# Optimization experiments

Hardware: AMD Instinct MI355X
Metric: run time of the kernel (lower is better)

## Reference

```python
import jax, jax.numpy as jnp
import numpy as np

B = 256   # batch size
NX = 256  # spatial grid points
T = 100   # time steps in u
TEMP = 1.0
LAM = 0.9  # lambda_1


def _advection(u, dt, dx, coeff):
    d = (jnp.roll(u, 1, axis=1) - jnp.roll(u, -1, axis=1)) * u
    return coeff[:, None, None] * dt[:, None, None] * d / (2.0 * dx[:, None, None])


def _diffusion(u, dt, dx, coeff):
    d = jnp.roll(u, 1, axis=1) + jnp.roll(u, -1, axis=1) - 2.0 * u
    return -(coeff[:, None, None] * dt[:, None, None] * d / dx[:, None, None] ** 2)


def _linear_advection(u, dt, dx, coeff):
    num = u - jnp.roll(u, -1, axis=1)
    return -coeff[:, None, None] * dt[:, None, None] * num / dx[:, None, None]


def _anchored_l2(xi, xj, ui, uj, dt, dx, coeff):
    # us[i, j, :] = ui[j, :, -1] - uj[i, :, -2]  -> [2B, 2B, NX]
    us = ui[..., -1][None, :, :] - uj[..., -2][:, None, :]
    adv = _advection(xi, dt, dx, coeff[:, 0])
    diff = _diffusion(xi, dt, dx, coeff[:, 1])
    dis = _linear_advection(xi, dt, dx, coeff[:, 2])
    updates = (adv + diff + dis)[..., 0]  # [2B, NX]
    pd = (xi[..., 0] + updates)[:, None, :] - xj[..., 0][None, :, :]  # [2B, 2B, NX]
    d = us - pd
    return jnp.sum(d * d, axis=-1)  # norm(dim=-1)**2


def reference(x1, x2, u, dt, dx, vs):
    bs = x1.shape[0]
    # _pde_similarity(vs): pairwise sqrt(sum|vi*vj|) / max(||vi||, ||vj||)
    prod = jnp.sqrt(jnp.sum(jnp.abs(vs[None, :, :] * vs[:, None, :]), axis=-1))
    nv = jnp.linalg.norm(vs, axis=-1)
    sim = prod / jnp.maximum(nv[:, None], nv[None, :])
    ss = jnp.nan_to_num(1.0 - LAM * sim, nan=0.0)
    # drop diagonal (row-major, static indices), then tile to [2B, 2(B-1)]
    ri, ci = np.nonzero(~np.eye(bs, dtype=bool))
    ss = ss[ri, ci].reshape(bs, bs - 1)
    ss = jnp.tile(ss, (2, 2))
    reps = jnp.concatenate([x2, x1], axis=0)           # [2B, NX, 1, 1]
    reps = reps.reshape(2 * bs, -1, reps.shape[-1])    # flatten(1,2) -> [2B, NX, 1]
    u2 = jnp.concatenate([u, u], axis=0)
    dt2 = jnp.concatenate([dt, dt], axis=0)
    vs2 = jnp.concatenate([vs, vs], axis=0)
    simmat = _anchored_l2(reps, reps, u2, u2, dt2, dx, vs2)  # [2B, 2B]
    l_pos = jnp.diagonal(simmat, offset=bs)
    r_pos = jnp.diagonal(simmat, offset=-bs)
    pos = jnp.concatenate([l_pos, r_pos]).reshape(2 * bs, 1)
    m = np.eye(2 * bs) + np.eye(2 * bs, k=-bs) + np.eye(2 * bs, k=bs)
    nri, nci = np.nonzero((1 - m).astype(bool))
    neg = simmat[nri, nci].reshape(2 * bs, 2 * bs - 2) * ss
    logits = jnp.concatenate([pos, neg], axis=1) / TEMP
    lp = jax.nn.log_softmax(logits, axis=-1)
    # CrossEntropyLoss(reduction='sum') with all labels == 0
    return -jnp.sum(lp[:, 0]) / (2 * bs)


def setup_inputs():
    key = jax.random.key(0)
    k1, k2, k3, k4, k5 = jax.random.split(key, 5)
    return {
        'x1': jax.random.normal(k1, (B, NX, 1, 1), dtype=jnp.float32),
        'x2': jax.random.normal(k2, (B, NX, 1, 1), dtype=jnp.float32),
        'u': jax.random.normal(k3, (B, NX, T), dtype=jnp.float32),
        'dt': jax.random.uniform(k4, (B,), dtype=jnp.float32),
        'dx': jnp.ones((1,), dtype=jnp.float32),
        'vs': jax.random.normal(k5, (B, 3), dtype=jnp.float32),
    }
```

## Files before the change

### kernel.cpp

```cpp
#include <hip/hip_runtime.h>
#include <math.h>

#define BQ 256
#define NXQ 256
#define TQ 100
#define N2 512
#define TILE 32
#define PITCH 257

__global__ __launch_bounds__(256) void prep_kernel(
    const float* __restrict__ x1, const float* __restrict__ x2,
    const float* __restrict__ u, const float* __restrict__ dt,
    const float* __restrict__ dx, const float* __restrict__ vs,
    float* __restrict__ A, float* __restrict__ C, float* __restrict__ SS) {
  int blk = blockIdx.x;
  int t = threadIdx.x;
  if (blk < N2) {
    int r = blk;
    int b = r & (BQ - 1);
    const float* xr = (r < BQ ? x2 : x1);
    __shared__ float ws[NXQ];
    ws[t] = xr[b * NXQ + t];
    __syncthreads();
    float w0 = ws[t];
    float wm = ws[(t + NXQ - 1) & (NXQ - 1)];
    float wp = ws[(t + 1) & (NXQ - 1)];
    float dtv = dt[b];
    float dxv = dx[0];
    float c0 = vs[b * 3 + 0], c1 = vs[b * 3 + 1], c2 = vs[b * 3 + 2];
    float adv = c0 * dtv * (wm - wp) * w0 / (2.0f * dxv);
    float dif = -(c1 * dtv * (wm + wp - 2.0f * w0) / (dxv * dxv));
    float dis = -c2 * dtv * (w0 - wp) / dxv;
    float upd = adv + dif + dis;
    const float* urow = u + (size_t)(b * NXQ + t) * TQ;
    A[r * NXQ + t] = urow[TQ - 1] + w0;
    C[r * NXQ + t] = urow[TQ - 2] + w0 + upd;
  } else {
    int i = blk - N2;
    int j = t;
    float vi0 = vs[i * 3], vi1 = vs[i * 3 + 1], vi2 = vs[i * 3 + 2];
    float vj0 = vs[j * 3], vj1 = vs[j * 3 + 1], vj2 = vs[j * 3 + 2];
    float nvi = sqrtf(vi0 * vi0 + vi1 * vi1 + vi2 * vi2);
    float nvj = sqrtf(vj0 * vj0 + vj1 * vj1 + vj2 * vj2);
    float prod = sqrtf(fabsf(vi0 * vj0) + fabsf(vi1 * vj1) + fabsf(vi2 * vj2));
    float sim = prod / fmaxf(nvi, nvj);
    float ssv = 1.0f - 0.9f * sim;
    if (isnan(ssv)) ssv = 0.0f;
    SS[i * BQ + j] = ssv;
  }
}

__global__ __launch_bounds__(256) void dist_kernel(const float* __restrict__ A,
                                                   const float* __restrict__ C,
                                                   float* __restrict__ SIM) {
  __shared__ float At[TILE * PITCH];
  __shared__ float Ct[TILE * PITCH];
  int t = threadIdx.x;
  int i0 = blockIdx.y * TILE;
  int j0 = blockIdx.x * TILE;
  for (int k = 0; k < TILE * NXQ / 256; k++) {
    int idx = k * 256 + t;
    int row = idx >> 8;
    int col = idx & (NXQ - 1);
    At[row * PITCH + col] = A[(j0 + row) * NXQ + col];
    Ct[row * PITCH + col] = C[(i0 + row) * NXQ + col];
  }
  __syncthreads();
  int ii = t >> 3;
  int jj = (t & 7) << 2;
  float acc0 = 0.f, acc1 = 0.f, acc2 = 0.f, acc3 = 0.f;
  for (int x = 0; x < NXQ; x++) {
    float cv = Ct[ii * PITCH + x];
    float d0 = At[(jj + 0) * PITCH + x] - cv;
    float d1 = At[(jj + 1) * PITCH + x] - cv;
    float d2 = At[(jj + 2) * PITCH + x] - cv;
    float d3 = At[(jj + 3) * PITCH + x] - cv;
    acc0 = fmaf(d0, d0, acc0);
    acc1 = fmaf(d1, d1, acc1);
    acc2 = fmaf(d2, d2, acc2);
    acc3 = fmaf(d3, d3, acc3);
  }
  float4 v = make_float4(acc0, acc1, acc2, acc3);
  *(float4*)&SIM[(i0 + ii) * N2 + j0 + jj] = v;
}

__global__ __launch_bounds__(256) void row_kernel(const float* __restrict__ SIM,
                                                  const float* __restrict__ SS,
                                                  double* __restrict__ ROW) {
  int r = blockIdx.x;
  int t = threadIdx.x;
  int rb = r & (BQ - 1);
  int jstar = (r + BQ) & (N2 - 1);
  float posval = SIM[r * N2 + jstar];
  float ssv = SS[rb * BQ + t];
  float v0, v1;
  {
    int j = t;
    if (j == jstar)                  v0 = posval;
    else if ((j & (BQ - 1)) == rb)   v0 = -INFINITY;
    else                             v0 = SIM[r * N2 + j] * ssv;
  }
  {
    int j = t + BQ;
    if (j == jstar)                  v1 = posval;
    else if ((j & (BQ - 1)) == rb)   v1 = -INFINITY;
    else                             v1 = SIM[r * N2 + j] * ssv;
  }
  float m = fmaxf(v0, v1);
  for (int off = 32; off > 0; off >>= 1) m = fmaxf(m, __shfl_down(m, off, 64));
  __shared__ float wmax[4];
  __shared__ double wsum[4];
  int wave = t >> 6, lane = t & 63;
  if (lane == 0) wmax[wave] = m;
  __syncthreads();
  float M = fmaxf(fmaxf(wmax[0], wmax[1]), fmaxf(wmax[2], wmax[3]));
  double s = 0.0;
  if (v0 != -INFINITY) s += exp((double)(v0 - M));
  if (v1 != -INFINITY) s += exp((double)(v1 - M));
  for (int off = 32; off > 0; off >>= 1) s += __shfl_down(s, off, 64);
  if (lane == 0) wsum[wave] = s;
  __syncthreads();
  if (t == 0) {
    double S = wsum[0] + wsum[1] + wsum[2] + wsum[3];
    ROW[r] = (double)M + log(S) - (double)posval;
  }
}

__global__ __launch_bounds__(256) void final_kernel(const double* __restrict__ ROW,
                                                    float* __restrict__ out) {
  int t = threadIdx.x;
  double s = ROW[t] + ROW[t + 256];
  for (int off = 32; off > 0; off >>= 1) s += __shfl_down(s, off, 64);
  __shared__ double wsum[4];
  int wave = t >> 6, lane = t & 63;
  if (lane == 0) wsum[wave] = s;
  __syncthreads();
  if (t == 0) {
    double S = wsum[0] + wsum[1] + wsum[2] + wsum[3];
    out[0] = (float)(S / (double)N2);
  }
}

extern "C" void kernel_launch(void* const* d_in, const int* in_sizes, int n_in,
                              void* d_out, int out_size, void* d_ws, size_t ws_size,
                              hipStream_t stream) {
  const float* x1 = (const float*)d_in[0];
  const float* x2 = (const float*)d_in[1];
  const float* u  = (const float*)d_in[2];
  const float* dt = (const float*)d_in[3];
  const float* dx = (const float*)d_in[4];
  const float* vs = (const float*)d_in[5];
  char* ws = (char*)d_ws;
  float*  SIM = (float*)(ws + 0);
  float*  A   = (float*)(ws + 1048576);
  float*  C   = (float*)(ws + 1572864);
  float*  SS  = (float*)(ws + 2097152);
  double* ROW = (double*)(ws + 2359296);
  float* out = (float*)d_out;

  prep_kernel<<<N2 + BQ, 256, 0, stream>>>(x1, x2, u, dt, dx, vs, A, C, SS);
  dim3 g2(N2 / TILE, N2 / TILE);
  dist_kernel<<<g2, 256, 0, stream>>>(A, C, SIM);
  row_kernel<<<N2, 256, 0, stream>>>(SIM, SS, ROW);
  final_kernel<<<1, 256, 0, stream>>>(ROW, out);
}
```

Baseline: 93.29 us.

## Restructure pipeline: fuse SS into row kernel, split-K dist tiles, atomic final reduction

After: 100.4 us. 1.08x slower.

```diff
diff --git a/kernel.cpp b/kernel.cpp
--- a/kernel.cpp
+++ b/kernel.cpp
@@ -5,111 +5,147 @@
 #define NXQ 256
 #define TQ 100
 #define N2 512
-#define TILE 32
-#define PITCH 257
+#define DPITCH 260
+#define PRP 17
 
 __global__ __launch_bounds__(256) void prep_kernel(
     const float* __restrict__ x1, const float* __restrict__ x2,
     const float* __restrict__ u, const float* __restrict__ dt,
     const float* __restrict__ dx, const float* __restrict__ vs,
-    float* __restrict__ A, float* __restrict__ C, float* __restrict__ SS) {
-  int blk = blockIdx.x;
+    float* __restrict__ A, float* __restrict__ C, unsigned* __restrict__ CNT) {
+  int b = blockIdx.x;
   int t = threadIdx.x;
-  if (blk < N2) {
-    int r = blk;
-    int b = r & (BQ - 1);
-    const float* xr = (r < BQ ? x2 : x1);
-    __shared__ float ws[NXQ];
-    ws[t] = xr[b * NXQ + t];
-    __syncthreads();
-    float w0 = ws[t];
-    float wm = ws[(t + NXQ - 1) & (NXQ - 1)];
-    float wp = ws[(t + 1) & (NXQ - 1)];
-    float dtv = dt[b];
-    float dxv = dx[0];
-    float c0 = vs[b * 3 + 0], c1 = vs[b * 3 + 1], c2 = vs[b * 3 + 2];
-    float adv = c0 * dtv * (wm - wp) * w0 / (2.0f * dxv);
-    float dif = -(c1 * dtv * (wm + wp - 2.0f * w0) / (dxv * dxv));
-    float dis = -c2 * dtv * (w0 - wp) / dxv;
-    float upd = adv + dif + dis;
-    const float* urow = u + (size_t)(b * NXQ + t) * TQ;
-    A[r * NXQ + t] = urow[TQ - 1] + w0;
-    C[r * NXQ + t] = urow[TQ - 2] + w0 + upd;
-  } else {
-    int i = blk - N2;
-    int j = t;
-    float vi0 = vs[i * 3], vi1 = vs[i * 3 + 1], vi2 = vs[i * 3 + 2];
-    float vj0 = vs[j * 3], vj1 = vs[j * 3 + 1], vj2 = vs[j * 3 + 2];
-    float nvi = sqrtf(vi0 * vi0 + vi1 * vi1 + vi2 * vi2);
-    float nvj = sqrtf(vj0 * vj0 + vj1 * vj1 + vj2 * vj2);
-    float prod = sqrtf(fabsf(vi0 * vj0) + fabsf(vi1 * vj1) + fabsf(vi2 * vj2));
-    float sim = prod / fmaxf(nvi, nvj);
-    float ssv = 1.0f - 0.9f * sim;
-    if (isnan(ssv)) ssv = 0.0f;
-    SS[i * BQ + j] = ssv;
-  }
-}
-
-__global__ __launch_bounds__(256) void dist_kernel(const float* __restrict__ A,
+  if (b == 0 && t == 0) *CNT = 0u;
+  __shared__ float w2s[NXQ], w1s[NXQ];
+  float w2 = x2[b * NXQ + t];
+  float w1 = x1[b * NXQ + t];
+  w2s[t] = w2;
+  w1s[t] = w1;
+  float2 uv = *(const float2*)(u + (size_t)(b * NXQ + t) * TQ + (TQ - 2));
+  float dtv = dt[b];
+  float dxv = dx[0];
+  float c0 = vs[b * 3 + 0], c1 = vs[b * 3 + 1], c2 = vs[b * 3 + 2];
+  __syncthreads();
+  int tm = (t + NXQ - 1) & (NXQ - 1);
+  int tp = (t + 1) & (NXQ - 1);
+  float w2m = w2s[tm], w2p = w2s[tp];
+  float w1m = w1s[tm], w1p = w1s[tp];
+  float adv2 = c0 * dtv * (w2m - w2p) * w2 / (2.0f * dxv);
+  float dif2 = -(c1 * dtv * (w2m + w2p - 2.0f * w2) / (dxv * dxv));
+  float dis2 = -c2 * dtv * (w2 - w2p) / dxv;
+  float adv1 = c0 * dtv * (w1m - w1p) * w1 / (2.0f * dxv);
+  float dif1 = -(c1 * dtv * (w1m + w1p - 2.0f * w1) / (dxv * dxv));
+  float dis1 = -c2 * dtv * (w1 - w1p) / dxv;
+  A[b * NXQ + t] = uv.y + w2;
+  A[(b + BQ) * NXQ + t] = uv.y + w1;
+  C[b * NXQ + t] = uv.x + w2 + (adv2 + dif2 + dis2);
+  C[(b + BQ) * NXQ + t] = uv.x + w1 + (adv1 + dif1 + dis1);
+}
+
+#define PAIR(P, Q, AV, CV)                                               \
+  {                                                                      \
+    float d0 = (AV).x - (CV).x, d1 = (AV).y - (CV).y;                    \
+    float d2 = (AV).z - (CV).z, d3 = (AV).w - (CV).w;                    \
+    acc[(P)*4 + (Q)] += fmaf(d0, d0, fmaf(d1, d1, fmaf(d2, d2, d3*d3))); \
+  }
+
+__global__ __launch_bounds__(512) void dist_kernel(const float* __restrict__ A,
                                                    const float* __restrict__ C,
                                                    float* __restrict__ SIM) {
-  __shared__ float At[TILE * PITCH];
-  __shared__ float Ct[TILE * PITCH];
+  __shared__ __align__(16) float At[32 * DPITCH];
+  __shared__ __align__(16) float Ct[32 * DPITCH];
+  __shared__ float PR[8 * 64 * PRP];
   int t = threadIdx.x;
-  int i0 = blockIdx.y * TILE;
-  int j0 = blockIdx.x * TILE;
-  for (int k = 0; k < TILE * NXQ / 256; k++) {
-    int idx = k * 256 + t;
-    int row = idx >> 8;
-    int col = idx & (NXQ - 1);
-    At[row * PITCH + col] = A[(j0 + row) * NXQ + col];
-    Ct[row * PITCH + col] = C[(i0 + row) * NXQ + col];
-  }
-  __syncthreads();
-  int ii = t >> 3;
-  int jj = (t & 7) << 2;
-  float acc0 = 0.f, acc1 = 0.f, acc2 = 0.f, acc3 = 0.f;
-  for (int x = 0; x < NXQ; x++) {
-    float cv = Ct[ii * PITCH + x];
-    float d0 = At[(jj + 0) * PITCH + x] - cv;
-    float d1 = At[(jj + 1) * PITCH + x] - cv;
-    float d2 = At[(jj + 2) * PITCH + x] - cv;
-    float d3 = At[(jj + 3) * PITCH + x] - cv;
-    acc0 = fmaf(d0, d0, acc0);
-    acc1 = fmaf(d1, d1, acc1);
-    acc2 = fmaf(d2, d2, acc2);
-    acc3 = fmaf(d3, d3, acc3);
-  }
-  float4 v = make_float4(acc0, acc1, acc2, acc3);
-  *(float4*)&SIM[(i0 + ii) * N2 + j0 + jj] = v;
+  int i0 = blockIdx.y * 32;
+  int j0 = blockIdx.x * 32;
+  for (int it = 0; it < 16; it++) {
+    int row = it * 2 + (t >> 8);
+    int col = t & 255;
+    int sw = ((row >> 2) & 7) << 2;
+    At[row * DPITCH + (col ^ sw)] = A[(j0 + row) * NXQ + col];
+    Ct[row * DPITCH + (col ^ sw)] = C[(i0 + row) * NXQ + col];
+  }
+  __syncthreads();
+  int w = t >> 6, ln = t & 63;
+  int ii = (ln >> 3) << 2;
+  int jj = (ln & 7) << 2;
+  int sa = ((jj >> 2) & 7) << 2;
+  int sc = ((ii >> 2) & 7) << 2;
+  const float* aB = &At[jj * DPITCH];
+  const float* cB = &Ct[ii * DPITCH];
+  float acc[16];
+#pragma unroll
+  for (int q = 0; q < 16; q++) acc[q] = 0.f;
+  int x0 = w * 32;
+#pragma unroll 2
+  for (int xi = 0; xi < 32; xi += 4) {
+    int xsa = (x0 + xi) ^ sa;
+    int xsc = (x0 + xi) ^ sc;
+    float4 a0 = *(const float4*)(aB + xsa);
+    float4 a1 = *(const float4*)(aB + DPITCH + xsa);
+    float4 a2 = *(const float4*)(aB + 2 * DPITCH + xsa);
+    float4 a3 = *(const float4*)(aB + 3 * DPITCH + xsa);
+    float4 cv0 = *(const float4*)(cB + xsc);
+    float4 cv1 = *(const float4*)(cB + DPITCH + xsc);
+    float4 cv2 = *(const float4*)(cB + 2 * DPITCH + xsc);
+    float4 cv3 = *(const float4*)(cB + 3 * DPITCH + xsc);
+    PAIR(0, 0, a0, cv0) PAIR(0, 1, a1, cv0) PAIR(0, 2, a2, cv0) PAIR(0, 3, a3, cv0)
+    PAIR(1, 0, a0, cv1) PAIR(1, 1, a1, cv1) PAIR(1, 2, a2, cv1) PAIR(1, 3, a3, cv1)
+    PAIR(2, 0, a0, cv2) PAIR(2, 1, a1, cv2) PAIR(2, 2, a2, cv2) PAIR(2, 3, a3, cv2)
+    PAIR(3, 0, a0, cv3) PAIR(3, 1, a1, cv3) PAIR(3, 2, a2, cv3) PAIR(3, 3, a3, cv3)
+  }
+#pragma unroll
+  for (int q = 0; q < 16; q++) PR[(w * 64 + ln) * PRP + q] = acc[q];
+  __syncthreads();
+  int li = t & 63;
+  int q0 = (t >> 6) * 2;
+  int iib = (li >> 3) << 2, jjb = (li & 7) << 2;
+  for (int qq = 0; qq < 2; qq++) {
+    int q = q0 + qq;
+    float s = 0.f;
+#pragma unroll
+    for (int pw = 0; pw < 8; pw++) s += PR[(pw * 64 + li) * PRP + q];
+    SIM[(i0 + iib + (q >> 2)) * N2 + (j0 + jjb + (q & 3))] = s;
+  }
 }
 
 __global__ __launch_bounds__(256) void row_kernel(const float* __restrict__ SIM,
-                                                  const float* __restrict__ SS,
-                                                  double* __restrict__ ROW) {
+                                                  const float* __restrict__ vs,
+                                                  double* __restrict__ ROW,
+                                                  unsigned* __restrict__ CNT,
+                                                  float* __restrict__ out) {
   int r = blockIdx.x;
   int t = threadIdx.x;
   int rb = r & (BQ - 1);
+  float vi0 = vs[rb * 3], vi1 = vs[rb * 3 + 1], vi2 = vs[rb * 3 + 2];
+  float vj0 = vs[t * 3], vj1 = vs[t * 3 + 1], vj2 = vs[t * 3 + 2];
+  float nvi = sqrtf(vi0 * vi0 + vi1 * vi1 + vi2 * vi2);
+  float nvj = sqrtf(vj0 * vj0 + vj1 * vj1 + vj2 * vj2);
+  float prod = sqrtf(fabsf(vi0 * vj0) + fabsf(vi1 * vj1) + fabsf(vi2 * vj2));
+  float sim = prod / fmaxf(nvi, nvj);
+  float ssv = 1.0f - 0.9f * sim;
+  if (isnan(ssv)) ssv = 0.0f;
+
   int jstar = (r + BQ) & (N2 - 1);
   float posval = SIM[r * N2 + jstar];
-  float ssv = SS[rb * BQ + t];
   float v0, v1;
   {
     int j = t;
-    if (j == jstar)                  v0 = posval;
-    else if ((j & (BQ - 1)) == rb)   v0 = -INFINITY;
-    else                             v0 = SIM[r * N2 + j] * ssv;
+    if (j == jstar)                v0 = posval;
+    else if ((j & (BQ - 1)) == rb) v0 = -INFINITY;
+    else                           v0 = SIM[r * N2 + j] * ssv;
   }
   {
     int j = t + BQ;
-    if (j == jstar)                  v1 = posval;
-    else if ((j & (BQ - 1)) == rb)   v1 = -INFINITY;
-    else                             v1 = SIM[r * N2 + j] * ssv;
+    if (j == jstar)                v1 = posval;
+    else if ((j & (BQ - 1)) == rb) v1 = -INFINITY;
+    else                           v1 = SIM[r * N2 + j] * ssv;
   }
   float m = fmaxf(v0, v1);
   for (int off = 32; off > 0; off >>= 1) m = fmaxf(m, __shfl_down(m, off, 64));
   __shared__ float wmax[4];
   __shared__ double wsum[4];
+  __shared__ int lastFlag;
   int wave = t >> 6, lane = t & 63;
   if (lane == 0) wmax[wave] = m;
   __syncthreads();
@@ -123,21 +159,21 @@
   if (t == 0) {
     double S = wsum[0] + wsum[1] + wsum[2] + wsum[3];
     ROW[r] = (double)M + log(S) - (double)posval;
-  }
-}
-
-__global__ __launch_bounds__(256) void final_kernel(const double* __restrict__ ROW,
-                                                    float* __restrict__ out) {
-  int t = threadIdx.x;
-  double s = ROW[t] + ROW[t + 256];
-  for (int off = 32; off > 0; off >>= 1) s += __shfl_down(s, off, 64);
-  __shared__ double wsum[4];
-  int wave = t >> 6, lane = t & 63;
-  if (lane == 0) wsum[wave] = s;
-  __syncthreads();
-  if (t == 0) {
-    double S = wsum[0] + wsum[1] + wsum[2] + wsum[3];
-    out[0] = (float)(S / (double)N2);
+    __threadfence();
+    unsigned old = atomicAdd(CNT, 1u);
+    int last = (old == N2 - 1) ? 1 : 0;
+    if (last) __threadfence();
+    lastFlag = last;
+  }
+  __syncthreads();
+  if (lastFlag) {
+    double sv = __hip_atomic_load(&ROW[t], __ATOMIC_RELAXED, __HIP_MEMORY_SCOPE_AGENT) +
+                __hip_atomic_load(&ROW[t + BQ], __ATOMIC_RELAXED, __HIP_MEMORY_SCOPE_AGENT);
+    for (int off = 32; off > 0; off >>= 1) sv += __shfl_down(sv, off, 64);
+    __shared__ double fsum[4];
+    if (lane == 0) fsum[wave] = sv;
+    __syncthreads();
+    if (t == 0) out[0] = (float)((fsum[0] + fsum[1] + fsum[2] + fsum[3]) / (double)N2);
   }
 }
 
@@ -151,16 +187,15 @@
   const float* dx = (const float*)d_in[4];
   const float* vs = (const float*)d_in[5];
   char* ws = (char*)d_ws;
-  float*  SIM = (float*)(ws + 0);
-  float*  A   = (float*)(ws + 1048576);
-  float*  C   = (float*)(ws + 1572864);
-  float*  SS  = (float*)(ws + 2097152);
-  double* ROW = (double*)(ws + 2359296);
+  float*    SIM = (float*)(ws + 0);
+  float*    A   = (float*)(ws + 1048576);
+  float*    C   = (float*)(ws + 1572864);
+  double*   ROW = (double*)(ws + 2097152);
+  unsigned* CNT = (unsigned*)(ws + 2101248);
   float* out = (float*)d_out;
 
-  prep_kernel<<<N2 + BQ, 256, 0, stream>>>(x1, x2, u, dt, dx, vs, A, C, SS);
-  dim3 g2(N2 / TILE, N2 / TILE);
-  dist_kernel<<<g2, 256, 0, stream>>>(A, C, SIM);
-  row_kernel<<<N2, 256, 0, stream>>>(SIM, SS, ROW);
-  final_kernel<<<1, 256, 0, stream>>>(ROW, out);
-}
+  prep_kernel<<<BQ, 256, 0, stream>>>(x1, x2, u, dt, dx, vs, A, C, CNT);
+  dim3 g2(N2 / 32, N2 / 32);
+  dist_kernel<<<g2, 512, 0, stream>>>(A, C, SIM);
+  row_kernel<<<N2, 256, 0, stream>>>(SIM, vs, ROW, CNT, out);
+}
```
